# Kernel tuning notes

Measured on AMD Instinct MI355X. Metric: run time of the kernel, lower is better.

The kernel has to match this reference:

```python
import jax, jax.numpy as jnp
import numpy as np
from jax import lax

B, H, W, C = 2, 96, 96, 96
D_STATE, D_CONV, EXPAND = 16, 3, 2
D_INNER = EXPAND * C            # 192 (VSSBlock inner width)
DM = D_INNER                    # Mamba d_model; Mamba expand=1 -> mamba d_inner == DM
DT_RANK = -(-DM // 16)          # ceil(192/16) = 12


def setup_inputs() -> dict:
    key = jax.random.key(0)
    ks = jax.random.split(key, 12)
    s = lambda k, shp, sc=0.02: jax.random.normal(k, shp, jnp.float32) * sc
    return {
        "x": jax.random.normal(ks[0], (B, H, W, C), jnp.float32),
        "norm_w": jnp.ones((C,), jnp.float32),
        "norm_b": jnp.zeros((C,), jnp.float32),
        "in_proj_w": s(ks[1], (C, 2 * D_INNER)),
        "conv2d_w": s(ks[2], (D_INNER, 1, D_CONV, D_CONV), 0.1),   # depthwise OIHW
        "m_in_proj_w": s(ks[3], (DM, 2 * DM)),
        "m_conv1d_w": s(ks[4], (DM, 1, D_CONV), 0.1),              # depthwise causal OIL
        "m_conv1d_b": jnp.zeros((DM,), jnp.float32),
        "m_x_proj_w": s(ks[5], (DM, DT_RANK + 2 * D_STATE)),
        "m_dt_proj_w": s(ks[6], (DT_RANK, DM), 0.1),
        "m_dt_proj_b": s(ks[7], (DM,), 0.1),
        "m_A_log": jnp.log(jnp.broadcast_to(
            jnp.arange(1, D_STATE + 1, dtype=jnp.float32), (DM, D_STATE))),
        "m_D": jnp.ones((DM,), jnp.float32),
        "m_out_proj_w": s(ks[8], (DM, DM)),
        "out_proj_w": s(ks[9], (D_INNER, C)),
    }


def _layernorm(x, w, b, eps=1e-5):
    mu = x.mean(-1, keepdims=True)
    var = jnp.mean(jnp.square(x - mu), -1, keepdims=True)
    return (x - mu) * lax.rsqrt(var + eps) * w + b


def _selective_scan(u, delta, A, Bm, Cm, Dv):
    # u, delta: (B,L,D); A: (D,N); Bm, Cm: (B,L,N); Dv: (D,)
    dA = jnp.exp(jnp.einsum('bld,dn->bldn', delta, A))           # (B,L,D,N)
    dBu = jnp.einsum('bld,bln->bldn', delta * u, Bm)             # (B,L,D,N)

    def step(h, inp):
        dA_t, dBu_t, C_t = inp
        h = dA_t * h + dBu_t                                      # (B,D,N)
        y = jnp.einsum('bdn,bn->bd', h, C_t)
        return h, y

    h0 = jnp.zeros((u.shape[0], A.shape[0], A.shape[1]), u.dtype)
    xs = (dA.transpose(1, 0, 2, 3), dBu.transpose(1, 0, 2, 3), Cm.transpose(1, 0, 2))
    _, ys = lax.scan(step, h0, xs)
    return ys.transpose(1, 0, 2) + u * Dv                         # (B,L,D)


def _mamba(seq, m_in_proj_w, m_conv1d_w, m_conv1d_b, m_x_proj_w,
           m_dt_proj_w, m_dt_proj_b, m_A_log, m_D, m_out_proj_w):
    # seq: (B,L,DM)
    xm, z = jnp.split(seq @ m_in_proj_w, 2, axis=-1)
    # causal depthwise conv1d over L
    xc = lax.conv_general_dilated(
        jnp.transpose(xm, (0, 2, 1)), m_conv1d_w, (1,), [(D_CONV - 1, 0)],
        feature_group_count=DM, dimension_numbers=('NCH', 'OIH', 'NCH'))
    xm = jax.nn.silu(jnp.transpose(xc + m_conv1d_b[None, :, None], (0, 2, 1)))
    x_dbl = xm @ m_x_proj_w
    dt, Bm, Cm = jnp.split(x_dbl, [DT_RANK, DT_RANK + D_STATE], axis=-1)
    delta = jax.nn.softplus(dt @ m_dt_proj_w + m_dt_proj_b)
    A = -jnp.exp(m_A_log)
    y = _selective_scan(xm, delta, A, Bm, Cm, m_D)
    return (y * jax.nn.silu(z)) @ m_out_proj_w


def reference(x, norm_w, norm_b, in_proj_w, conv2d_w, m_in_proj_w, m_conv1d_w,
              m_conv1d_b, m_x_proj_w, m_dt_proj_w, m_dt_proj_b, m_A_log, m_D,
              m_out_proj_w, out_proj_w):
    Bsz, Hh, Ww, _ = x.shape
    xn = _layernorm(x, norm_w, norm_b)
    x_in, x_gate = jnp.split(xn @ in_proj_w, 2, axis=-1)          # (B,H,W,D_INNER) x2
    # depthwise 3x3 conv, 'same' padding
    xc = lax.conv_general_dilated(
        jnp.transpose(x_in, (0, 3, 1, 2)), conv2d_w, (1, 1), [(1, 1), (1, 1)],
        feature_group_count=D_INNER, dimension_numbers=('NCHW', 'OIHW', 'NCHW'))
    xc = jax.nn.silu(jnp.transpose(xc, (0, 2, 3, 1)))
    seq = xc.reshape(Bsz, Hh * Ww, D_INNER)
    y = _mamba(seq, m_in_proj_w, m_conv1d_w, m_conv1d_b, m_x_proj_w,
               m_dt_proj_w, m_dt_proj_b, m_A_log, m_D, m_out_proj_w)
    y = y.reshape(Bsz, Hh, Ww, D_INNER) * jax.nn.silu(x_gate)
    return x + y @ out_proj_w
```

## Files before the change

kernel.cpp:

```cpp
#include <hip/hip_runtime.h>

#define DEV_INLINE __device__ __forceinline__

constexpr int BATCH = 2;
constexpr int HH = 96, WW = 96, CC = 96;
constexpr int DI = 192;
constexpr int NS = 16;
constexpr int LSEQ = HH * WW;
constexpr int TT = BATCH * LSEQ;
constexpr int CHUNK = 16;
constexpr int NCHUNK = LSEQ / CHUNK;
constexpr int SUP = 24, NSUP = NCHUNK / SUP;
constexpr int QDN = DI * NS;

typedef __attribute__((ext_vector_type(8))) short bf16x8;
typedef __attribute__((ext_vector_type(4))) float f32x4;

DEV_INLINE float silu_f(float x) { return x / (1.f + __expf(-x)); }
DEV_INLINE float softplus_f(float x) {
  return fmaxf(x, 0.f) + log1pf(__expf(-fabsf(x)));
}
DEV_INLINE ushort f2bf(float f) {
  union { float f; unsigned u; } c; c.f = f;
  unsigned u = c.u + 0x7FFF + ((c.u >> 16) & 1);
  return (ushort)(u >> 16);
}
DEV_INLINE float bf2f(ushort u) {
  union { unsigned u; float f; } c; c.u = ((unsigned)u) << 16; return c.f;
}

__global__ __launch_bounds__(256)
void castw_kernel(const float* __restrict__ w0, const float* __restrict__ w1,
                  const float* __restrict__ w2, const float* __restrict__ w3,
                  const float* __restrict__ wx, const float* __restrict__ wdt,
                  const float* __restrict__ wc1,
                  ushort* __restrict__ t0, ushort* __restrict__ t1,
                  ushort* __restrict__ t2, ushort* __restrict__ t3,
                  ushort* __restrict__ t4, ushort* __restrict__ t5,
                  float* __restrict__ cwT)
{
  int id = blockIdx.x * 256 + threadIdx.x;
  if (id < 36864) {
    int k = id / 384, n = id % 384;
    t0[n * 96 + k] = f2bf(w0[id]);
  } else if (id < 110592) {
    int j = id - 36864; int k = j / 384, n = j % 384;
    t1[n * 192 + k] = f2bf(w1[j]);
  } else if (id < 147456) {
    int j = id - 110592; int k = j / 192, n = j % 192;
    t2[n * 192 + k] = f2bf(w2[j]);
  } else if (id < 165888) {
    int j = id - 147456; int k = j / 96, n = j % 96;
    t3[n * 192 + k] = f2bf(w3[j]);
  } else if (id < 172032) {
    int j = id - 165888;
    t3[96 * 192 + j] = 0;
  } else if (id < 180480) {
    int j = id - 172032; int k = j / 44, c = j % 44;
    int r = (c < 12) ? (32 + c) : (c < 28 ? (c - 12) : (16 + c - 28));
    t4[r * 192 + k] = f2bf(wx[j]);
  } else if (id < 181248) {
    int j = id - 180480;
    t4[44 * 192 + j] = 0;
  } else if (id < 183552) {
    int j = id - 181248; int r = j / 192, d = j % 192;
    t5[d * 32 + r] = f2bf(wdt[j]);
  } else if (id < 187392) {
    int j = id - 183552; int d = j / 20, r = 12 + j % 20;
    t5[d * 32 + r] = 0;
  } else if (id < 187968) {
    int j = id - 187392; int d = j / 3, k = j % 3;
    cwT[k * 192 + d] = wc1[j];
  }
}

__global__ __launch_bounds__(256)
void ln_inproj_kernel(const float* __restrict__ x, const float* __restrict__ nw,
                      const float* __restrict__ nbias, const ushort* __restrict__ Wt0,
                      ushort* __restrict__ xz0)
{
  __shared__ ushort sA[128][104];
  const int tid = threadIdx.x;
  const int m0 = blockIdx.x * 128;
  const int n0 = blockIdx.y * 64;
  {
    const int tok = tid >> 1, h = tid & 1;
    const float* xr = x + (size_t)(m0 + tok) * 96 + h * 48;
    float v[48];
    float s = 0.f, ss = 0.f;
#pragma unroll
    for (int i = 0; i < 12; ++i) {
      float4 t4 = *(const float4*)(xr + i * 4);
      v[i*4+0] = t4.x; v[i*4+1] = t4.y; v[i*4+2] = t4.z; v[i*4+3] = t4.w;
      s += (t4.x + t4.y) + (t4.z + t4.w);
      ss += (t4.x*t4.x + t4.y*t4.y) + (t4.z*t4.z + t4.w*t4.w);
    }
    s += __shfl_xor(s, 1);
    ss += __shfl_xor(ss, 1);
    float mean = s * (1.f/96.f);
    float var = ss * (1.f/96.f) - mean*mean;
    float rstd = rsqrtf(var + 1e-5f);
    const float* wr = nw + h*48;
    const float* br = nbias + h*48;
#pragma unroll
    for (int i = 0; i < 12; ++i) {
      float4 w4 = *(const float4*)(wr + i*4);
      float4 b4 = *(const float4*)(br + i*4);
      unsigned p0 = (unsigned)f2bf((v[i*4+0]-mean)*rstd*w4.x + b4.x)
                  | ((unsigned)f2bf((v[i*4+1]-mean)*rstd*w4.y + b4.y) << 16);
      unsigned p1 = (unsigned)f2bf((v[i*4+2]-mean)*rstd*w4.z + b4.z)
                  | ((unsigned)f2bf((v[i*4+3]-mean)*rstd*w4.w + b4.w) << 16);
      unsigned* dst = (unsigned*)&sA[tok][h*48 + i*4];
      dst[0] = p0; dst[1] = p1;
    }
  }
  __syncthreads();

  const int wid = tid >> 6, lane = tid & 63;
  const int wm = wid >> 1, wn = wid & 1;
  const int l16 = lane & 15, quad = lane >> 4;
  const f32x4 z4 = {0.f, 0.f, 0.f, 0.f};
  f32x4 acc[4][2];
#pragma unroll
  for (int i = 0; i < 4; ++i)
#pragma unroll
    for (int j = 0; j < 2; ++j) acc[i][j] = z4;

#pragma unroll
  for (int k0 = 0; k0 < 96; k0 += 32) {
    bf16x8 xf[4], wf[2];
#pragma unroll
    for (int i = 0; i < 4; ++i)
      xf[i] = *(const bf16x8*)&sA[wm*64 + i*16 + l16][k0 + quad*8];
#pragma unroll
    for (int j = 0; j < 2; ++j)
      wf[j] = *(const bf16x8*)(Wt0 + (size_t)(n0 + wn*32 + j*16 + l16) * 96 + k0 + quad*8);
#pragma unroll
    for (int i = 0; i < 4; ++i)
#pragma unroll
      for (int j = 0; j < 2; ++j)
        acc[i][j] = __builtin_amdgcn_mfma_f32_16x16x32_bf16(wf[j], xf[i], acc[i][j], 0, 0, 0);
  }
#pragma unroll
  for (int i = 0; i < 4; ++i) {
    const int token = m0 + wm*64 + i*16 + l16;
#pragma unroll
    for (int j = 0; j < 2; ++j) {
      const int nb = n0 + wn*32 + j*16 + quad*4;
      ushort4 o;
      o.x = f2bf(acc[i][j][0]); o.y = f2bf(acc[i][j][1]);
      o.z = f2bf(acc[i][j][2]); o.w = f2bf(acc[i][j][3]);
      *(ushort4*)(xz0 + (size_t)token * 384 + nb) = o;
    }
  }
}

__global__ __launch_bounds__(256)
void conv2d_silu_kernel(const ushort* __restrict__ xz0, const float* __restrict__ w,
                        ushort* __restrict__ xc)
{
  __shared__ float ws[DI * 9];
  for (int i = threadIdx.x; i < DI * 9; i += 256) ws[i] = w[i];
  __syncthreads();
  int id = blockIdx.x * 256 + threadIdx.x;
  int dq = id % 48;
  int p  = id / 48;
  int j = p % WW;
  int i = (p / WW) % HH;
  int b = p / (WW * HH);
  int d = dq * 4;
  float a0 = 0.f, a1 = 0.f, a2 = 0.f, a3 = 0.f;
#pragma unroll
  for (int ki = 0; ki < 3; ++ki) {
    int ii = i + ki - 1;
    if (ii < 0 || ii >= HH) continue;
#pragma unroll
    for (int kj = 0; kj < 3; ++kj) {
      int jj = j + kj - 1;
      if (jj < 0 || jj >= WW) continue;
      const ushort4 v = *(const ushort4*)(xz0 + ((size_t)((b * HH + ii) * WW + jj)) * 384 + d);
      int wk = ki * 3 + kj;
      a0 = fmaf(bf2f(v.x), ws[(d + 0) * 9 + wk], a0);
      a1 = fmaf(bf2f(v.y), ws[(d + 1) * 9 + wk], a1);
      a2 = fmaf(bf2f(v.z), ws[(d + 2) * 9 + wk], a2);
      a3 = fmaf(bf2f(v.w), ws[(d + 3) * 9 + wk], a3);
    }
  }
  ushort4 o;
  o.x = f2bf(silu_f(a0)); o.y = f2bf(silu_f(a1));
  o.z = f2bf(silu_f(a2)); o.w = f2bf(silu_f(a3));
  *(ushort4*)(xc + (size_t)p * DI + d) = o;
}

__global__ __launch_bounds__(256)
void mfma_gemm_kernel(const ushort* __restrict__ A, int lda,
                      const ushort* __restrict__ Bt, int ldb,
                      ushort* __restrict__ Cout, int ldc, int K)
{
  const int tid = threadIdx.x;
  const int wid = tid >> 6, lane = tid & 63;
  const int wm = wid >> 1, wn = wid & 1;
  const int m0 = blockIdx.x * 128 + wm * 64;
  const int n0 = blockIdx.y * 64 + wn * 32;
  const int l16 = lane & 15, quad = lane >> 4;

  f32x4 acc[4][2];
  const f32x4 z4 = {0.f, 0.f, 0.f, 0.f};
#pragma unroll
  for (int i = 0; i < 4; ++i)
#pragma unroll
    for (int j = 0; j < 2; ++j) acc[i][j] = z4;

  for (int k0 = 0; k0 < K; k0 += 32) {
    bf16x8 xf[4], wf[2];
#pragma unroll
    for (int i = 0; i < 4; ++i)
      xf[i] = *(const bf16x8*)(A + (size_t)(m0 + i * 16 + l16) * lda + k0 + quad * 8);
#pragma unroll
    for (int j = 0; j < 2; ++j)
      wf[j] = *(const bf16x8*)(Bt + (size_t)(n0 + j * 16 + l16) * ldb + k0 + quad * 8);
#pragma unroll
    for (int i = 0; i < 4; ++i)
#pragma unroll
      for (int j = 0; j < 2; ++j)
        acc[i][j] = __builtin_amdgcn_mfma_f32_16x16x32_bf16(wf[j], xf[i], acc[i][j], 0, 0, 0);
  }
#pragma unroll
  for (int i = 0; i < 4; ++i) {
    const int token = m0 + i * 16 + l16;
#pragma unroll
    for (int j = 0; j < 2; ++j) {
      const int nb = n0 + j * 16 + quad * 4;
      ushort4 o;
      o.x = f2bf(acc[i][j][0]); o.y = f2bf(acc[i][j][1]);
      o.z = f2bf(acc[i][j][2]); o.w = f2bf(acc[i][j][3]);
      *(ushort4*)(Cout + (size_t)token * ldc + nb) = o;
    }
  }
}

__global__ __launch_bounds__(256)
void mprep_kernel(const ushort* __restrict__ xz1, const float* __restrict__ cwT,
                  const float* __restrict__ cb, const ushort* __restrict__ Wxt,
                  const ushort* __restrict__ Wdtt, const float* __restrict__ bdt,
                  const float* __restrict__ Alog,
                  ushort* __restrict__ xmb, ushort* __restrict__ dlt,
                  float* __restrict__ bc, unsigned* __restrict__ PE)
{
  __shared__ ushort sxm[32][204];
  __shared__ ushort sdlt[32][204];
  __shared__ float sbc[32][36];
  const int tid = threadIdx.x;
  const int bid = blockIdx.x;
  const int T0 = bid * 32;
  const f32x4 z4 = {0.f, 0.f, 0.f, 0.f};

  for (int task = tid; task < 1536; task += 256) {
    int dq = task % 48, tok = task / 48;
    int t = T0 + tok, l = t % LSEQ;
    int d = dq * 4;
    float4 b4 = *(const float4*)(cb + d);
    float a0 = b4.x, a1 = b4.y, a2 = b4.z, a3 = b4.w;
#pragma unroll
    for (int k = 0; k < 3; ++k) {
      if (l + k - 2 < 0) continue;
      const ushort4 v = *(const ushort4*)(xz1 + (size_t)(t + k - 2) * 384 + d);
      const float4 w4 = *(const float4*)(cwT + k * 192 + d);
      a0 = fmaf(bf2f(v.x), w4.x, a0);
      a1 = fmaf(bf2f(v.y), w4.y, a1);
      a2 = fmaf(bf2f(v.z), w4.z, a2);
      a3 = fmaf(bf2f(v.w), w4.w, a3);
    }
    ushort4 o;
    o.x = f2bf(silu_f(a0)); o.y = f2bf(silu_f(a1));
    o.z = f2bf(silu_f(a2)); o.w = f2bf(silu_f(a3));
    *(ushort4*)&sxm[tok][d] = o;
    *(ushort4*)(xmb + (size_t)t * DI + d) = o;
  }
  __syncthreads();

  {
    const int wv = tid >> 6, lane = tid & 63;
    const int l16 = lane & 15, quad = lane >> 4;
    const int s = wv & 1, role = wv >> 1;
    const int tokb = s * 16;
    if (role == 0) {
      f32x4 aB = z4, aC = z4;
#pragma unroll
      for (int k0 = 0; k0 < 192; k0 += 32) {
        bf16x8 uf = *(const bf16x8*)&sxm[tokb + l16][k0 + quad * 8];
        bf16x8 wB = *(const bf16x8*)(Wxt + (size_t)(l16) * 192 + k0 + quad * 8);
        bf16x8 wC = *(const bf16x8*)(Wxt + (size_t)(16 + l16) * 192 + k0 + quad * 8);
        aB = __builtin_amdgcn_mfma_f32_16x16x32_bf16(wB, uf, aB, 0, 0, 0);
        aC = __builtin_amdgcn_mfma_f32_16x16x32_bf16(wC, uf, aC, 0, 0, 0);
      }
      float4 vB = make_float4(aB[0], aB[1], aB[2], aB[3]);
      float4 vC = make_float4(aC[0], aC[1], aC[2], aC[3]);
      *(float4*)&sbc[tokb + l16][quad * 4] = vB;
      *(float4*)&sbc[tokb + l16][16 + quad * 4] = vC;
      *(float4*)(bc + (size_t)(T0 + tokb + l16) * 32 + quad * 4) = vB;
      *(float4*)(bc + (size_t)(T0 + tokb + l16) * 32 + 16 + quad * 4) = vC;
    } else {
      f32x4 aD = z4;
#pragma unroll
      for (int k0 = 0; k0 < 192; k0 += 32) {
        bf16x8 uf = *(const bf16x8*)&sxm[tokb + l16][k0 + quad * 8];
        bf16x8 wD = *(const bf16x8*)(Wxt + (size_t)(32 + l16) * 192 + k0 + quad * 8);
        aD = __builtin_amdgcn_mfma_f32_16x16x32_bf16(wD, uf, aD, 0, 0, 0);
      }
      bf16x8 dtf;
#pragma unroll
      for (int j = 0; j < 8; ++j) {
        int n = quad * 8 + j;
        int src = ((n >> 2) & 3) * 16 + l16;
        float tv = __shfl(aD[j & 3], src);
        dtf[j] = (short)((n < 16) ? f2bf(tv) : (ushort)0);
      }
      f32x4 a2[12];
#pragma unroll
      for (int jj = 0; jj < 12; ++jj) {
        bf16x8 wf = *(const bf16x8*)(Wdtt + (size_t)(jj * 16 + l16) * 32 + quad * 8);
        a2[jj] = __builtin_amdgcn_mfma_f32_16x16x32_bf16(wf, dtf, z4, 0, 0, 0);
      }
#pragma unroll
      for (int jj = 0; jj < 12; ++jj) {
        const int nb = jj * 16 + quad * 4;
        const float4 b4 = *(const float4*)(bdt + nb);
        ushort4 o;
        o.x = f2bf(softplus_f(a2[jj][0] + b4.x));
        o.y = f2bf(softplus_f(a2[jj][1] + b4.y));
        o.z = f2bf(softplus_f(a2[jj][2] + b4.z));
        o.w = f2bf(softplus_f(a2[jj][3] + b4.w));
        *(ushort4*)&sdlt[tokb + l16][nb] = o;
        *(ushort4*)(dlt + (size_t)(T0 + tokb + l16) * DI + nb) = o;
      }
    }
  }
  __syncthreads();

  for (int task = tid; task < 384; task += 256) {
    const int d = task % 192, c = task / 192;
    float Av[16];
#pragma unroll
    for (int j = 0; j < 16; ++j) Av[j] = -__expf(Alog[d * 16 + j]);
    float e[16];
#pragma unroll
    for (int j = 0; j < 16; ++j) e[j] = 0.f;
    float sdl = 0.f;
    for (int l = 0; l < CHUNK; ++l) {
      const int tl = c * 16 + l;
      float dl = bf2f(sdlt[tl][d]);
      float u  = bf2f(sxm[tl][d]);
      const float4 B0 = *(const float4*)&sbc[tl][0];
      const float4 B1 = *(const float4*)&sbc[tl][4];
      const float4 B2 = *(const float4*)&sbc[tl][8];
      const float4 B3 = *(const float4*)&sbc[tl][12];
      const float Bv[16] = {B0.x, B0.y, B0.z, B0.w, B1.x, B1.y, B1.z, B1.w,
                            B2.x, B2.y, B2.z, B2.w, B3.x, B3.y, B3.z, B3.w};
      float du = dl * u;
      sdl += dl;
#pragma unroll
      for (int j = 0; j < 16; ++j) {
        float a = __expf(dl * Av[j]);
        e[j] = fmaf(a, e[j], du * Bv[j]);
      }
    }
    const int batch = bid / 288;
    const int gci = (bid % 288) * 2 + c;
    size_t base = ((size_t)(batch * NCHUNK + gci)) * QDN + d;
#pragma unroll
    for (int j = 0; j < 16; ++j) {
      unsigned p = f2bf(__expf(Av[j] * sdl));
      unsigned ev = f2bf(e[j]);
      PE[base + j * 192] = (p << 16) | ev;
    }
  }
}

__global__ __launch_bounds__(256)
void scan2a_kernel(const unsigned* __restrict__ PE,
                   float* __restrict__ SP, float* __restrict__ SE)
{
  int id = blockIdx.x * 256 + threadIdx.x;
  int q = id % QDN;
  int s = (id / QDN) % NSUP;
  int b = id / (QDN * NSUP);
  float cp = 1.f, ce = 0.f;
#pragma unroll 6
  for (int c = 0; c < SUP; ++c) {
    unsigned pe = PE[((size_t)(b * NCHUNK + s * SUP + c)) * QDN + q];
    float p = bf2f((ushort)(pe >> 16));
    float e = bf2f((ushort)(pe & 0xFFFF));
    ce = fmaf(p, ce, e);
    cp *= p;
  }
  SP[id] = cp; SE[id] = ce;
}

__global__ __launch_bounds__(256)
void scan2b_kernel(const float* __restrict__ SP, const float* __restrict__ SE,
                   float* __restrict__ Hsup)
{
  int id = blockIdx.x * 256 + threadIdx.x;
  int q = id % QDN;
  int b = id / QDN;
  float carry = 0.f;
#pragma unroll
  for (int s = 0; s < NSUP; ++s) {
    size_t idx = ((size_t)(b * NSUP + s)) * QDN + q;
    Hsup[idx] = carry;
    carry = fmaf(SP[idx], carry, SE[idx]);
  }
}

__global__ __launch_bounds__(256)
void scan2c_kernel(const unsigned* __restrict__ PE, const float* __restrict__ Hsup,
                   ushort* __restrict__ Hin)
{
  int id = blockIdx.x * 256 + threadIdx.x;
  int q = id % QDN;
  int s = (id / QDN) % NSUP;
  int b = id / (QDN * NSUP);
  float h = Hsup[id];
#pragma unroll 6
  for (int c = 0; c < SUP; ++c) {
    size_t idx = ((size_t)(b * NCHUNK + s * SUP + c)) * QDN + q;
    Hin[idx] = f2bf(h);
    unsigned pe = PE[idx];
    float p = bf2f((ushort)(pe >> 16));
    float e = bf2f((ushort)(pe & 0xFFFF));
    h = fmaf(p, h, e);
  }
}

__global__ __launch_bounds__(192)
void scan3_kernel(const ushort* __restrict__ dlt, const ushort* __restrict__ xmb,
                  const float* __restrict__ bc, const float* __restrict__ Alog,
                  const float* __restrict__ Dv, const ushort* __restrict__ xz1,
                  const ushort* __restrict__ Hin, ushort* __restrict__ yout)
{
  __shared__ float sBC[CHUNK][32];
  const int d = threadIdx.x;
  const int g = blockIdx.x % NCHUNK;
  const int b = blockIdx.x / NCHUNK;
  const int t0 = b * LSEQ + g * CHUNK;
  for (int i = threadIdx.x; i < CHUNK * 32; i += 192) {
    int l = i >> 5, j = i & 31;
    sBC[l][j] = bc[(size_t)(t0 + l) * 32 + j];
  }
  float Av[16];
#pragma unroll
  for (int j = 0; j < 16; ++j) Av[j] = -__expf(Alog[d * 16 + j]);
  const float Dd = Dv[d];
  float h[16];
  {
    size_t hb = ((size_t)(b * NCHUNK + g)) * QDN + d;
#pragma unroll
    for (int j = 0; j < 16; ++j) h[j] = bf2f(Hin[hb + j * 192]);
  }
  __syncthreads();
#pragma unroll 4
  for (int l = 0; l < CHUNK; ++l) {
    const int t = t0 + l;
    float dl = bf2f(dlt[(size_t)t * DI + d]);
    float u  = bf2f(xmb[(size_t)t * DI + d]);
    float z  = bf2f(xz1[(size_t)t * 384 + 192 + d]);
    float du = dl * u;
    float y0 = 0.f, y1 = 0.f, y2 = 0.f, y3 = 0.f;
#pragma unroll
    for (int j = 0; j < 16; ++j) {
      float a = __expf(dl * Av[j]);
      h[j] = fmaf(a, h[j], du * sBC[l][j]);
      float hc = h[j] * sBC[l][16 + j];
      if ((j & 3) == 0) y0 += hc;
      else if ((j & 3) == 1) y1 += hc;
      else if ((j & 3) == 2) y2 += hc;
      else y3 += hc;
    }
    float y = (y0 + y1) + (y2 + y3) + u * Dd;
    yout[(size_t)t * DI + d] = f2bf(y * silu_f(z));
  }
}

__global__ __launch_bounds__(256)
void outproj_kernel(const ushort* __restrict__ yfin, const ushort* __restrict__ Wt2,
                    const ushort* __restrict__ xz0, const ushort* __restrict__ Wt3,
                    const float* __restrict__ x, float* __restrict__ out)
{
  __shared__ ushort yg_s[32][204];
  const int tid = threadIdx.x;
  const int wid = tid >> 6, lane = tid & 63;
  const int wm = wid >> 1, wn = wid & 1;
  const int l16 = lane & 15, quad = lane >> 4;
  const int m0 = blockIdx.x * 32;
  const f32x4 z4 = {0.f, 0.f, 0.f, 0.f};

  f32x4 acc[6];
#pragma unroll
  for (int j = 0; j < 6; ++j) acc[j] = z4;
  const int mt = m0 + wm * 16 + l16;
#pragma unroll
  for (int k0 = 0; k0 < 192; k0 += 32) {
    bf16x8 af = *(const bf16x8*)(yfin + (size_t)mt * 192 + k0 + quad * 8);
#pragma unroll
    for (int nj = 0; nj < 6; ++nj) {
      bf16x8 wf = *(const bf16x8*)(Wt2 + (size_t)(wn * 96 + nj * 16 + l16) * 192 + k0 + quad * 8);
      acc[nj] = __builtin_amdgcn_mfma_f32_16x16x32_bf16(wf, af, acc[nj], 0, 0, 0);
    }
  }
#pragma unroll
  for (int nj = 0; nj < 6; ++nj) {
    const int tok = wm * 16 + l16;
    const int nb = wn * 96 + nj * 16 + quad * 4;
    const ushort4 g4 = *(const ushort4*)(xz0 + (size_t)(m0 + tok) * 384 + 192 + nb);
    float v0 = acc[nj][0] * silu_f(bf2f(g4.x));
    float v1 = acc[nj][1] * silu_f(bf2f(g4.y));
    float v2 = acc[nj][2] * silu_f(bf2f(g4.z));
    float v3 = acc[nj][3] * silu_f(bf2f(g4.w));
    unsigned p0 = (unsigned)f2bf(v0) | ((unsigned)f2bf(v1) << 16);
    unsigned p1 = (unsigned)f2bf(v2) | ((unsigned)f2bf(v3) << 16);
    unsigned* dst = (unsigned*)&yg_s[tok][nb];
    dst[0] = p0; dst[1] = p1;
  }
  __syncthreads();

  f32x4 acc2[3];
#pragma unroll
  for (int j = 0; j < 3; ++j) acc2[j] = z4;
#pragma unroll
  for (int k0 = 0; k0 < 192; k0 += 32) {
    bf16x8 af = *(const bf16x8*)&yg_s[wm * 16 + l16][k0 + quad * 8];
#pragma unroll
    for (int nj = 0; nj < 3; ++nj) {
      bf16x8 wf = *(const bf16x8*)(Wt3 + (size_t)(wn * 48 + nj * 16 + l16) * 192 + k0 + quad * 8);
      acc2[nj] = __builtin_amdgcn_mfma_f32_16x16x32_bf16(wf, af, acc2[nj], 0, 0, 0);
    }
  }
#pragma unroll
  for (int nj = 0; nj < 3; ++nj) {
    const int tok = wm * 16 + l16;
    const int nb = wn * 48 + nj * 16 + quad * 4;
    const float4 r4 = *(const float4*)(x + (size_t)(m0 + tok) * 96 + nb);
    *(float4*)(out + (size_t)(m0 + tok) * 96 + nb) =
        make_float4(acc2[nj][0] + r4.x, acc2[nj][1] + r4.y,
                    acc2[nj][2] + r4.z, acc2[nj][3] + r4.w);
  }
}

extern "C" void kernel_launch(void* const* d_in, const int* in_sizes, int n_in,
                              void* d_out, int out_size, void* d_ws, size_t ws_size,
                              hipStream_t stream)
{
  const float* x         = (const float*)d_in[0];
  const float* norm_w    = (const float*)d_in[1];
  const float* norm_b    = (const float*)d_in[2];
  const float* in_proj_w = (const float*)d_in[3];
  const float* conv2d_w  = (const float*)d_in[4];
  const float* m_in_proj = (const float*)d_in[5];
  const float* m_c1d_w   = (const float*)d_in[6];
  const float* m_c1d_b   = (const float*)d_in[7];
  const float* m_x_proj  = (const float*)d_in[8];
  const float* m_dt_w    = (const float*)d_in[9];
  const float* m_dt_b    = (const float*)d_in[10];
  const float* m_A_log   = (const float*)d_in[11];
  const float* m_D       = (const float*)d_in[12];
  const float* m_out_w   = (const float*)d_in[13];
  const float* out_w     = (const float*)d_in[14];
  float* out = (float*)d_out;

  char* wp = (char*)d_ws;
  auto alloc = [&](size_t bytes) {
    char* r = wp; wp += (bytes + 255) & ~(size_t)255; return r;
  };
  ushort* Wt0    = (ushort*)alloc(36864 * 2);
  ushort* Wt1    = (ushort*)alloc(73728 * 2);
  ushort* Wt2    = (ushort*)alloc(36864 * 2);
  ushort* Wt3    = (ushort*)alloc(24576 * 2);
  ushort* Wxt    = (ushort*)alloc(9216 * 2);
  ushort* Wdtt   = (ushort*)alloc(6144 * 2);
  float*  cw1T   = (float*)alloc(576 * 4);
  ushort* xz0    = (ushort*)alloc((size_t)TT * 384 * 2);
  ushort* xc_bf  = (ushort*)alloc((size_t)TT * 192 * 2);
  ushort* xz1    = (ushort*)alloc((size_t)TT * 384 * 2);
  ushort* xmb_bf = (ushort*)alloc((size_t)TT * 192 * 2);
  float*  bc     = (float*)alloc((size_t)TT * 32 * 4);
  ushort* dlt    = (ushort*)alloc((size_t)TT * 192 * 2);
  unsigned* PE   = (unsigned*)alloc((size_t)BATCH * NCHUNK * QDN * 4);
  float*  SP     = (float*)alloc((size_t)BATCH * NSUP * QDN * 4);
  float*  SE     = (float*)alloc((size_t)BATCH * NSUP * QDN * 4);
  float*  Hsup   = (float*)alloc((size_t)BATCH * NSUP * QDN * 4);
  ushort* Hin    = (ushort*)alloc((size_t)BATCH * NCHUNK * QDN * 2);
  ushort* yfin   = (ushort*)alloc((size_t)TT * 192 * 2);

  castw_kernel<<<735, 256, 0, stream>>>(in_proj_w, m_in_proj, m_out_w, out_w,
                                        m_x_proj, m_dt_w, m_c1d_w,
                                        Wt0, Wt1, Wt2, Wt3, Wxt, Wdtt, cw1T);
  ln_inproj_kernel<<<dim3(TT / 128, 6), 256, 0, stream>>>(x, norm_w, norm_b, Wt0, xz0);
  conv2d_silu_kernel<<<TT * 48 / 256, 256, 0, stream>>>(xz0, conv2d_w, xc_bf);
  mfma_gemm_kernel<<<dim3(TT / 128, 6), 256, 0, stream>>>(xc_bf, 192, Wt1, 192, xz1, 384, 192);
  mprep_kernel<<<TT / 32, 256, 0, stream>>>(xz1, cw1T, m_c1d_b, Wxt, Wdtt, m_dt_b,
                                            m_A_log, xmb_bf, dlt, bc, PE);
  scan2a_kernel<<<BATCH * NSUP * QDN / 256, 256, 0, stream>>>(PE, SP, SE);
  scan2b_kernel<<<BATCH * QDN / 256, 256, 0, stream>>>(SP, SE, Hsup);
  scan2c_kernel<<<BATCH * NSUP * QDN / 256, 256, 0, stream>>>(PE, Hsup, Hin);
  scan3_kernel<<<BATCH * NCHUNK, 192, 0, stream>>>(dlt, xmb_bf, bc, m_A_log, m_D, xz1, Hin, yfin);
  outproj_kernel<<<TT / 32, 256, 0, stream>>>(yfin, Wt2, xz0, Wt3, x, out);
}
```

Measured before the change: 237.1 us.

## Rebalance mprep kernel across six waves with staged dt projection

Raises the mprep block from 256 to 384 threads (6 waves). Each wave now computes one 16-wide slice of x_proj (B, C or dt), and the dt_proj matmul is split across three column groups after a shared-memory handoff of the dt values. The per-chunk scan loop maps one task per thread and is partially unrolled. The goal is to remove the load imbalance where the dt waves did far more serial MFMA and softplus work, and to leave no threads idle in the chunk scan. In exchange it adds an extra barrier and a small shared buffer, and may raise register pressure.

```diff
diff --git a/kernel.cpp b/kernel.cpp
--- a/kernel.cpp
+++ b/kernel.cpp
@@ -239,7 +239,7 @@
   }
 }
 
-__global__ __launch_bounds__(256)
+__global__ __launch_bounds__(384)
 void mprep_kernel(const ushort* __restrict__ xz1, const float* __restrict__ cwT,
                   const float* __restrict__ cb, const ushort* __restrict__ Wxt,
                   const ushort* __restrict__ Wdtt, const float* __restrict__ bdt,
@@ -249,13 +249,16 @@
 {
   __shared__ ushort sxm[32][204];
   __shared__ ushort sdlt[32][204];
+  __shared__ ushort sdtf[32][16];
   __shared__ float sbc[32][36];
   const int tid = threadIdx.x;
   const int bid = blockIdx.x;
   const int T0 = bid * 32;
   const f32x4 z4 = {0.f, 0.f, 0.f, 0.f};
 
-  for (int task = tid; task < 1536; task += 256) {
+#pragma unroll
+  for (int it = 0; it < 4; ++it) {
+    int task = tid + it * 384;
     int dq = task % 48, tok = task / 48;
     int t = T0 + tok, l = t % LSEQ;
     int d = dq * 4;
@@ -279,67 +282,66 @@
   }
   __syncthreads();
 
+  const int wv = tid >> 6, lane = tid & 63;
+  const int l16 = lane & 15, quad = lane >> 4;
+
   {
-    const int wv = tid >> 6, lane = tid & 63;
-    const int l16 = lane & 15, quad = lane >> 4;
-    const int s = wv & 1, role = wv >> 1;
+    const int s = wv / 3, role = wv % 3;
     const int tokb = s * 16;
-    if (role == 0) {
-      f32x4 aB = z4, aC = z4;
-#pragma unroll
-      for (int k0 = 0; k0 < 192; k0 += 32) {
-        bf16x8 uf = *(const bf16x8*)&sxm[tokb + l16][k0 + quad * 8];
-        bf16x8 wB = *(const bf16x8*)(Wxt + (size_t)(l16) * 192 + k0 + quad * 8);
-        bf16x8 wC = *(const bf16x8*)(Wxt + (size_t)(16 + l16) * 192 + k0 + quad * 8);
-        aB = __builtin_amdgcn_mfma_f32_16x16x32_bf16(wB, uf, aB, 0, 0, 0);
-        aC = __builtin_amdgcn_mfma_f32_16x16x32_bf16(wC, uf, aC, 0, 0, 0);
-      }
-      float4 vB = make_float4(aB[0], aB[1], aB[2], aB[3]);
-      float4 vC = make_float4(aC[0], aC[1], aC[2], aC[3]);
-      *(float4*)&sbc[tokb + l16][quad * 4] = vB;
-      *(float4*)&sbc[tokb + l16][16 + quad * 4] = vC;
-      *(float4*)(bc + (size_t)(T0 + tokb + l16) * 32 + quad * 4) = vB;
-      *(float4*)(bc + (size_t)(T0 + tokb + l16) * 32 + 16 + quad * 4) = vC;
+    f32x4 acc = z4;
+#pragma unroll
+    for (int k0 = 0; k0 < 192; k0 += 32) {
+      bf16x8 uf = *(const bf16x8*)&sxm[tokb + l16][k0 + quad * 8];
+      bf16x8 wf = *(const bf16x8*)(Wxt + (size_t)(role * 16 + l16) * 192 + k0 + quad * 8);
+      acc = __builtin_amdgcn_mfma_f32_16x16x32_bf16(wf, uf, acc, 0, 0, 0);
+    }
+    if (role < 2) {
+      float4 v = make_float4(acc[0], acc[1], acc[2], acc[3]);
+      *(float4*)&sbc[tokb + l16][role * 16 + quad * 4] = v;
+      *(float4*)(bc + (size_t)(T0 + tokb + l16) * 32 + role * 16 + quad * 4) = v;
     } else {
-      f32x4 aD = z4;
-#pragma unroll
-      for (int k0 = 0; k0 < 192; k0 += 32) {
-        bf16x8 uf = *(const bf16x8*)&sxm[tokb + l16][k0 + quad * 8];
-        bf16x8 wD = *(const bf16x8*)(Wxt + (size_t)(32 + l16) * 192 + k0 + quad * 8);
-        aD = __builtin_amdgcn_mfma_f32_16x16x32_bf16(wD, uf, aD, 0, 0, 0);
-      }
-      bf16x8 dtf;
-#pragma unroll
-      for (int j = 0; j < 8; ++j) {
-        int n = quad * 8 + j;
-        int src = ((n >> 2) & 3) * 16 + l16;
-        float tv = __shfl(aD[j & 3], src);
-        dtf[j] = (short)((n < 16) ? f2bf(tv) : (ushort)0);
-      }
-      f32x4 a2[12];
-#pragma unroll
-      for (int jj = 0; jj < 12; ++jj) {
-        bf16x8 wf = *(const bf16x8*)(Wdtt + (size_t)(jj * 16 + l16) * 32 + quad * 8);
-        a2[jj] = __builtin_amdgcn_mfma_f32_16x16x32_bf16(wf, dtf, z4, 0, 0, 0);
-      }
-#pragma unroll
-      for (int jj = 0; jj < 12; ++jj) {
-        const int nb = jj * 16 + quad * 4;
-        const float4 b4 = *(const float4*)(bdt + nb);
-        ushort4 o;
-        o.x = f2bf(softplus_f(a2[jj][0] + b4.x));
-        o.y = f2bf(softplus_f(a2[jj][1] + b4.y));
-        o.z = f2bf(softplus_f(a2[jj][2] + b4.z));
-        o.w = f2bf(softplus_f(a2[jj][3] + b4.w));
-        *(ushort4*)&sdlt[tokb + l16][nb] = o;
-        *(ushort4*)(dlt + (size_t)(T0 + tokb + l16) * DI + nb) = o;
-      }
+      ushort4 o;
+      o.x = f2bf(acc[0]); o.y = f2bf(acc[1]);
+      o.z = f2bf(acc[2]); o.w = f2bf(acc[3]);
+      *(ushort4*)&sdtf[tokb + l16][quad * 4] = o;
     }
   }
   __syncthreads();
 
-  for (int task = tid; task < 384; task += 256) {
-    const int d = task % 192, c = task / 192;
+  {
+    const int s = wv / 3, cg = wv % 3;
+    const int tokb = s * 16;
+    bf16x8 dtf;
+    if (quad < 2) {
+      uint4 v = *(const uint4*)&sdtf[tokb + l16][quad * 8];
+      dtf = *(bf16x8*)&v;
+    } else {
+#pragma unroll
+      for (int j = 0; j < 8; ++j) dtf[j] = 0;
+    }
+    f32x4 a2[4];
+#pragma unroll
+    for (int jj = 0; jj < 4; ++jj) {
+      bf16x8 wf = *(const bf16x8*)(Wdtt + (size_t)(cg * 64 + jj * 16 + l16) * 32 + quad * 8);
+      a2[jj] = __builtin_amdgcn_mfma_f32_16x16x32_bf16(wf, dtf, z4, 0, 0, 0);
+    }
+#pragma unroll
+    for (int jj = 0; jj < 4; ++jj) {
+      const int nb = cg * 64 + jj * 16 + quad * 4;
+      const float4 b4 = *(const float4*)(bdt + nb);
+      ushort4 o;
+      o.x = f2bf(softplus_f(a2[jj][0] + b4.x));
+      o.y = f2bf(softplus_f(a2[jj][1] + b4.y));
+      o.z = f2bf(softplus_f(a2[jj][2] + b4.z));
+      o.w = f2bf(softplus_f(a2[jj][3] + b4.w));
+      *(ushort4*)&sdlt[tokb + l16][nb] = o;
+      *(ushort4*)(dlt + (size_t)(T0 + tokb + l16) * DI + nb) = o;
+    }
+  }
+  __syncthreads();
+
+  {
+    const int d = tid % 192, c = tid / 192;
     float Av[16];
 #pragma unroll
     for (int j = 0; j < 16; ++j) Av[j] = -__expf(Alog[d * 16 + j]);
@@ -347,6 +349,7 @@
 #pragma unroll
     for (int j = 0; j < 16; ++j) e[j] = 0.f;
     float sdl = 0.f;
+#pragma unroll 4
     for (int l = 0; l < CHUNK; ++l) {
       const int tl = c * 16 + l;
       float dl = bf2f(sdlt[tl][d]);
@@ -598,7 +601,7 @@
   ln_inproj_kernel<<<dim3(TT / 128, 6), 256, 0, stream>>>(x, norm_w, norm_b, Wt0, xz0);
   conv2d_silu_kernel<<<TT * 48 / 256, 256, 0, stream>>>(xz0, conv2d_w, xc_bf);
   mfma_gemm_kernel<<<dim3(TT / 128, 6), 256, 0, stream>>>(xc_bf, 192, Wt1, 192, xz1, 384, 192);
-  mprep_kernel<<<TT / 32, 256, 0, stream>>>(xz1, cw1T, m_c1d_b, Wxt, Wdtt, m_dt_b,
+  mprep_kernel<<<TT / 32, 384, 0, stream>>>(xz1, cw1T, m_c1d_b, Wxt, Wdtt, m_dt_b,
                                             m_A_log, xmb_bf, dlt, bc, PE);
   scan2a_kernel<<<BATCH * NSUP * QDN / 256, 256, 0, stream>>>(PE, SP, SE);
   scan2b_kernel<<<BATCH * QDN / 256, 256, 0, stream>>>(SP, SE, Hsup);
```

Result: no change. 240.9 us (+1.6%).

## Fuse selective-scan output stage with gated output projections

Applied to the files above, without the earlier changes.

Merges the final scan kernel and the output-projection kernel so each 16-token chunk's scan result stays in shared memory and feeds the two MFMA GEMMs directly. This removes the intermediate y buffer round trip through global memory and one launch. In exchange, each block now covers only 16 tokens, so the projection weights are reloaded by twice as many blocks. The fourth wave also idles during the scan phase.

```diff
diff --git a/kernel.cpp b/kernel.cpp
--- a/kernel.cpp
+++ b/kernel.cpp
@@ -331,7 +331,7 @@
         o.y = f2bf(softplus_f(a2[jj][1] + b4.y));
         o.z = f2bf(softplus_f(a2[jj][2] + b4.z));
         o.w = f2bf(softplus_f(a2[jj][3] + b4.w));
-        *(ushort4*)&sdlt[tokb + l16][nb] = o;
+        *(ushort4*)&sdlt[l16 + tokb][nb] = o;
         *(ushort4*)(dlt + (size_t)(T0 + tokb + l16) * DI + nb) = o;
       }
     }
@@ -433,117 +433,111 @@
   }
 }
 
-__global__ __launch_bounds__(192)
-void scan3_kernel(const ushort* __restrict__ dlt, const ushort* __restrict__ xmb,
-                  const float* __restrict__ bc, const float* __restrict__ Alog,
-                  const float* __restrict__ Dv, const ushort* __restrict__ xz1,
-                  const ushort* __restrict__ Hin, ushort* __restrict__ yout)
+__global__ __launch_bounds__(256)
+void scan3_outproj_kernel(const ushort* __restrict__ dlt, const ushort* __restrict__ xmb,
+                          const float* __restrict__ bc, const float* __restrict__ Alog,
+                          const float* __restrict__ Dv, const ushort* __restrict__ xz1,
+                          const ushort* __restrict__ Hin, const ushort* __restrict__ xz0,
+                          const ushort* __restrict__ Wt2, const ushort* __restrict__ Wt3,
+                          const float* __restrict__ x, float* __restrict__ out)
 {
   __shared__ float sBC[CHUNK][32];
-  const int d = threadIdx.x;
+  __shared__ ushort sY[16][204];
+  __shared__ ushort sYG[16][204];
+  const int tid = threadIdx.x;
   const int g = blockIdx.x % NCHUNK;
   const int b = blockIdx.x / NCHUNK;
   const int t0 = b * LSEQ + g * CHUNK;
-  for (int i = threadIdx.x; i < CHUNK * 32; i += 192) {
+  const f32x4 z4 = {0.f, 0.f, 0.f, 0.f};
+
+  for (int i = tid; i < CHUNK * 32; i += 256) {
     int l = i >> 5, j = i & 31;
     sBC[l][j] = bc[(size_t)(t0 + l) * 32 + j];
   }
-  float Av[16];
-#pragma unroll
-  for (int j = 0; j < 16; ++j) Av[j] = -__expf(Alog[d * 16 + j]);
-  const float Dd = Dv[d];
-  float h[16];
+  if (tid < 192) {
+    const int d = tid;
+    float Av[16];
+#pragma unroll
+    for (int j = 0; j < 16; ++j) Av[j] = -__expf(Alog[d * 16 + j]);
+    const float Dd = Dv[d];
+    float h[16];
+    {
+      size_t hb = ((size_t)(b * NCHUNK + g)) * QDN + d;
+#pragma unroll
+      for (int j = 0; j < 16; ++j) h[j] = bf2f(Hin[hb + j * 192]);
+    }
+    __syncthreads();
+#pragma unroll 4
+    for (int l = 0; l < CHUNK; ++l) {
+      const int t = t0 + l;
+      float dl = bf2f(dlt[(size_t)t * DI + d]);
+      float u  = bf2f(xmb[(size_t)t * DI + d]);
+      float z  = bf2f(xz1[(size_t)t * 384 + 192 + d]);
+      float du = dl * u;
+      float y0 = 0.f, y1 = 0.f, y2 = 0.f, y3 = 0.f;
+#pragma unroll
+      for (int j = 0; j < 16; ++j) {
+        float a = __expf(dl * Av[j]);
+        h[j] = fmaf(a, h[j], du * sBC[l][j]);
+        float hc = h[j] * sBC[l][16 + j];
+        if ((j & 3) == 0) y0 += hc;
+        else if ((j & 3) == 1) y1 += hc;
+        else if ((j & 3) == 2) y2 += hc;
+        else y3 += hc;
+      }
+      float y = (y0 + y1) + (y2 + y3) + u * Dd;
+      sY[l][d] = f2bf(y * silu_f(z));
+    }
+  } else {
+    __syncthreads();
+  }
+  __syncthreads();
+
+  const int wv = tid >> 6, lane = tid & 63;
+  const int l16 = lane & 15, quad = lane >> 4;
+  const int token = t0 + l16;
+
   {
-    size_t hb = ((size_t)(b * NCHUNK + g)) * QDN + d;
-#pragma unroll
-    for (int j = 0; j < 16; ++j) h[j] = bf2f(Hin[hb + j * 192]);
+    f32x4 acc1[3] = {z4, z4, z4};
+#pragma unroll
+    for (int k0 = 0; k0 < 192; k0 += 32) {
+      bf16x8 af = *(const bf16x8*)&sY[l16][k0 + quad * 8];
+#pragma unroll
+      for (int i = 0; i < 3; ++i) {
+        const int tt = wv + i * 4;
+        bf16x8 wf = *(const bf16x8*)(Wt2 + (size_t)(tt * 16 + l16) * 192 + k0 + quad * 8);
+        acc1[i] = __builtin_amdgcn_mfma_f32_16x16x32_bf16(wf, af, acc1[i], 0, 0, 0);
+      }
+    }
+#pragma unroll
+    for (int i = 0; i < 3; ++i) {
+      const int nb = (wv + i * 4) * 16 + quad * 4;
+      const ushort4 g4 = *(const ushort4*)(xz0 + (size_t)token * 384 + 192 + nb);
+      unsigned p0 = (unsigned)f2bf(acc1[i][0] * silu_f(bf2f(g4.x)))
+                  | ((unsigned)f2bf(acc1[i][1] * silu_f(bf2f(g4.y))) << 16);
+      unsigned p1 = (unsigned)f2bf(acc1[i][2] * silu_f(bf2f(g4.z)))
+                  | ((unsigned)f2bf(acc1[i][3] * silu_f(bf2f(g4.w))) << 16);
+      unsigned* dst = (unsigned*)&sYG[l16][nb];
+      dst[0] = p0; dst[1] = p1;
+    }
   }
   __syncthreads();
-#pragma unroll 4
-  for (int l = 0; l < CHUNK; ++l) {
-    const int t = t0 + l;
-    float dl = bf2f(dlt[(size_t)t * DI + d]);
-    float u  = bf2f(xmb[(size_t)t * DI + d]);
-    float z  = bf2f(xz1[(size_t)t * 384 + 192 + d]);
-    float du = dl * u;
-    float y0 = 0.f, y1 = 0.f, y2 = 0.f, y3 = 0.f;
-#pragma unroll
-    for (int j = 0; j < 16; ++j) {
-      float a = __expf(dl * Av[j]);
-      h[j] = fmaf(a, h[j], du * sBC[l][j]);
-      float hc = h[j] * sBC[l][16 + j];
-      if ((j & 3) == 0) y0 += hc;
-      else if ((j & 3) == 1) y1 += hc;
-      else if ((j & 3) == 2) y2 += hc;
-      else y3 += hc;
-    }
-    float y = (y0 + y1) + (y2 + y3) + u * Dd;
-    yout[(size_t)t * DI + d] = f2bf(y * silu_f(z));
-  }
-}
-
-__global__ __launch_bounds__(256)
-void outproj_kernel(const ushort* __restrict__ yfin, const ushort* __restrict__ Wt2,
-                    const ushort* __restrict__ xz0, const ushort* __restrict__ Wt3,
-                    const float* __restrict__ x, float* __restrict__ out)
-{
-  __shared__ ushort yg_s[32][204];
-  const int tid = threadIdx.x;
-  const int wid = tid >> 6, lane = tid & 63;
-  const int wm = wid >> 1, wn = wid & 1;
-  const int l16 = lane & 15, quad = lane >> 4;
-  const int m0 = blockIdx.x * 32;
-  const f32x4 z4 = {0.f, 0.f, 0.f, 0.f};
-
-  f32x4 acc[6];
-#pragma unroll
-  for (int j = 0; j < 6; ++j) acc[j] = z4;
-  const int mt = m0 + wm * 16 + l16;
-#pragma unroll
-  for (int k0 = 0; k0 < 192; k0 += 32) {
-    bf16x8 af = *(const bf16x8*)(yfin + (size_t)mt * 192 + k0 + quad * 8);
-#pragma unroll
-    for (int nj = 0; nj < 6; ++nj) {
-      bf16x8 wf = *(const bf16x8*)(Wt2 + (size_t)(wn * 96 + nj * 16 + l16) * 192 + k0 + quad * 8);
-      acc[nj] = __builtin_amdgcn_mfma_f32_16x16x32_bf16(wf, af, acc[nj], 0, 0, 0);
-    }
-  }
-#pragma unroll
-  for (int nj = 0; nj < 6; ++nj) {
-    const int tok = wm * 16 + l16;
-    const int nb = wn * 96 + nj * 16 + quad * 4;
-    const ushort4 g4 = *(const ushort4*)(xz0 + (size_t)(m0 + tok) * 384 + 192 + nb);
-    float v0 = acc[nj][0] * silu_f(bf2f(g4.x));
-    float v1 = acc[nj][1] * silu_f(bf2f(g4.y));
-    float v2 = acc[nj][2] * silu_f(bf2f(g4.z));
-    float v3 = acc[nj][3] * silu_f(bf2f(g4.w));
-    unsigned p0 = (unsigned)f2bf(v0) | ((unsigned)f2bf(v1) << 16);
-    unsigned p1 = (unsigned)f2bf(v2) | ((unsigned)f2bf(v3) << 16);
-    unsigned* dst = (unsigned*)&yg_s[tok][nb];
-    dst[0] = p0; dst[1] = p1;
-  }
-  __syncthreads();
-
-  f32x4 acc2[3];
-#pragma unroll
-  for (int j = 0; j < 3; ++j) acc2[j] = z4;
-#pragma unroll
-  for (int k0 = 0; k0 < 192; k0 += 32) {
-    bf16x8 af = *(const bf16x8*)&yg_s[wm * 16 + l16][k0 + quad * 8];
-#pragma unroll
-    for (int nj = 0; nj < 3; ++nj) {
-      bf16x8 wf = *(const bf16x8*)(Wt3 + (size_t)(wn * 48 + nj * 16 + l16) * 192 + k0 + quad * 8);
-      acc2[nj] = __builtin_amdgcn_mfma_f32_16x16x32_bf16(wf, af, acc2[nj], 0, 0, 0);
-    }
-  }
-#pragma unroll
-  for (int nj = 0; nj < 3; ++nj) {
-    const int tok = wm * 16 + l16;
-    const int nb = wn * 48 + nj * 16 + quad * 4;
-    const float4 r4 = *(const float4*)(x + (size_t)(m0 + tok) * 96 + nb);
-    *(float4*)(out + (size_t)(m0 + tok) * 96 + nb) =
-        make_float4(acc2[nj][0] + r4.x, acc2[nj][1] + r4.y,
-                    acc2[nj][2] + r4.z, acc2[nj][3] + r4.w);
+
+#pragma unroll
+  for (int rep = 0; rep < 2; ++rep) {
+    const int tt = wv + rep * 4;
+    if (tt >= 6) break;
+    f32x4 acc2 = z4;
+#pragma unroll
+    for (int k0 = 0; k0 < 192; k0 += 32) {
+      bf16x8 af = *(const bf16x8*)&sYG[l16][k0 + quad * 8];
+      bf16x8 wf = *(const bf16x8*)(Wt3 + (size_t)(tt * 16 + l16) * 192 + k0 + quad * 8);
+      acc2 = __builtin_amdgcn_mfma_f32_16x16x32_bf16(wf, af, acc2, 0, 0, 0);
+    }
+    const int nb = tt * 16 + quad * 4;
+    const float4 r4 = *(const float4*)(x + (size_t)token * 96 + nb);
+    *(float4*)(out + (size_t)token * 96 + nb) =
+        make_float4(acc2[0] + r4.x, acc2[1] + r4.y, acc2[2] + r4.z, acc2[3] + r4.w);
   }
 }
 
@@ -590,7 +584,6 @@
   float*  SE     = (float*)alloc((size_t)BATCH * NSUP * QDN * 4);
   float*  Hsup   = (float*)alloc((size_t)BATCH * NSUP * QDN * 4);
   ushort* Hin    = (ushort*)alloc((size_t)BATCH * NCHUNK * QDN * 2);
-  ushort* yfin   = (ushort*)alloc((size_t)TT * 192 * 2);
 
   castw_kernel<<<735, 256, 0, stream>>>(in_proj_w, m_in_proj, m_out_w, out_w,
                                         m_x_proj, m_dt_w, m_c1d_w,
@@ -603,6 +596,6 @@
   scan2a_kernel<<<BATCH * NSUP * QDN / 256, 256, 0, stream>>>(PE, SP, SE);
   scan2b_kernel<<<BATCH * QDN / 256, 256, 0, stream>>>(SP, SE, Hsup);
   scan2c_kernel<<<BATCH * NSUP * QDN / 256, 256, 0, stream>>>(PE, Hsup, Hin);
-  scan3_kernel<<<BATCH * NCHUNK, 192, 0, stream>>>(dlt, xmb_bf, bc, m_A_log, m_D, xz1, Hin, yfin);
-  outproj_kernel<<<TT / 32, 256, 0, stream>>>(yfin, Wt2, xz0, Wt3, x, out);
-}
+  scan3_outproj_kernel<<<BATCH * NCHUNK, 256, 0, stream>>>(
+      dlt, xmb_bf, bc, m_A_log, m_D, xz1, Hin, xz0, Wt2, Wt3, x, out);
+}
```

Result: faster. 229.2 us (-3.3%).
